# Performance work log

Hardware: AMD Instinct MI355X
Metric: run time of the kernel (lower is better)

## Reference

```python
import jax, jax.numpy as jnp
import numpy as np

N = 4096      # n_nodes
F = 512       # input_dim
R = 64        # repr_dim
H = 8         # n_heads
EPS_BIAS = 0.01
ALPHA = 0.2   # LeakyReLU negative slope
NEG_BIG = 1e16


def setup_inputs() -> dict:
    key = jax.random.key(0)
    k1, k2, k3, k4, k5 = jax.random.split(key, 5)
    node_matrix = jax.random.normal(k1, (N, F), dtype=jnp.float32)
    adjacency_matrix = (jax.random.uniform(k2, (N, N)) < 0.01).astype(jnp.float32)
    adjacency_matrix = jnp.maximum(adjacency_matrix, jnp.eye(N, dtype=jnp.float32))
    # learned parameters (xavier-ish scale)
    W = jax.random.normal(k3, (H, F, R), dtype=jnp.float32) * 0.06
    shared_attention = jax.random.normal(k4, (H, 2 * R), dtype=jnp.float32) * 0.1
    attention_biases = jax.random.normal(k5, (N, N), dtype=jnp.float32) * 0.02
    return {
        "node_matrix": node_matrix,
        "adjacency_matrix": adjacency_matrix,
        "W": W,
        "shared_attention": shared_attention,
        "attention_biases": attention_biases,
    }


def reference(node_matrix, adjacency_matrix, W, shared_attention, attention_biases):
    # hidden_repr: [H, N, R]
    hidden = jnp.einsum('nf,hfr->hnr', node_matrix, W)
    # per-head source/destination scores: [H, N]
    a_src = jnp.einsum('hnr,hr->hn', hidden, shared_attention[:, :R])
    a_dst = jnp.einsum('hnr,hr->hn', hidden, shared_attention[:, R:])
    # broadcast-sum + trainable pair bias: [H, N, N]
    pre = a_src[:, :, None] + a_dst[:, None, :] + EPS_BIAS * attention_biases[None]
    full = jnp.where(pre >= 0, pre, ALPHA * pre)  # LeakyReLU
    # adjacency masking then row softmax
    scores = full + (-NEG_BIG * (1.0 - adjacency_matrix))[None]
    att = jax.nn.softmax(scores, axis=-1)  # [H, N, N]
    # weighted aggregation: [H, N, R]
    out = jnp.einsum('hnm,hmr->hnr', att, hidden)
    # 'concat' aggregation: [N, H*R], head h occupies columns h*R:(h+1)*R
    return jnp.transpose(out, (1, 0, 2)).reshape(N, H * R)
```

## Files before the change

kernel.cpp:

```cpp
#include <hip/hip_runtime.h>
#include <hip/hip_bf16.h>

#define NN 4096
#define FF 512
#define RR 64
#define HH 8
#define HR (HH * RR)
#define CAP 128
#define ATT_STRIDE 144

typedef short bf16x8 __attribute__((ext_vector_type(8)));
typedef float f32x4 __attribute__((ext_vector_type(4)));

__device__ __forceinline__ unsigned short f2bf(float f) {
  __hip_bfloat16 h = __float2bfloat16(f);
  return *reinterpret_cast<unsigned short*>(&h);
}
__device__ __forceinline__ float bf2f(unsigned short u) {
  union { unsigned u32; float f; } cv;
  cv.u32 = ((unsigned)u) << 16;
  return cv.f;
}
__device__ __forceinline__ unsigned nib4(const float4 v) {
  unsigned m = 0;
  if (v.x != 0.f) m |= 1u;
  if (v.y != 0.f) m |= 2u;
  if (v.z != 0.f) m |= 4u;
  if (v.w != 0.f) m |= 8u;
  return m;
}

__global__ __launch_bounds__(256) void k_stream(
    const float* __restrict__ X, const float* __restrict__ W,
    const float* __restrict__ adj,
    unsigned short* __restrict__ Xb, unsigned short* __restrict__ BbT,
    int* __restrict__ colsG, int* __restrict__ cnts)
{
  __shared__ unsigned short wt[64][68];
  const int b = blockIdx.x;
  const int tid = threadIdx.x;

  if (b < 1024) {
    const int lane = tid & 63;
    const int row = b * 4 + (tid >> 6);
    const float* arow = adj + (size_t)row * NN;
    unsigned long long pm = 0;
    {
      float4 buf[8];
#pragma unroll
      for (int c = 0; c < 8; ++c)
        buf[c] = *reinterpret_cast<const float4*>(&arow[c * 256 + (lane << 2)]);
#pragma unroll
      for (int c = 0; c < 8; ++c)
        pm |= (unsigned long long)nib4(buf[c]) << (4 * c);
#pragma unroll
      for (int c = 0; c < 8; ++c)
        buf[c] = *reinterpret_cast<const float4*>(&arow[(c + 8) * 256 + (lane << 2)]);
#pragma unroll
      for (int c = 0; c < 8; ++c)
        pm |= (unsigned long long)nib4(buf[c]) << (4 * c + 32);
    }
    const int cnt = __popcll(pm);
    int pfx = cnt;
#pragma unroll
    for (int off = 1; off < 64; off <<= 1) {
      const int o = __shfl_up(pfx, off);
      if (lane >= off) pfx += o;
    }
    int pos = pfx - cnt;
    unsigned long long m = pm;
    int* cg = colsG + (size_t)row * CAP;
    while (m) {
      const int bit = (int)__builtin_ctzll(m);
      m &= m - 1;
      if (pos < CAP) cg[pos] = ((bit >> 2) << 8) + (lane << 2) + (bit & 3);
      ++pos;
    }
    const int tot = __shfl(pfx, 63);
    for (int p = tot + lane; p < CAP; p += 64) cg[p] = 0;
    if (lane == 63) cnts[row] = tot < CAP ? tot : CAP;
  } else if (b < 3072) {
    const int t = (b - 1024) * 256 + tid;
    const float4 v = reinterpret_cast<const float4*>(X)[t];
    ushort4 u;
    u.x = f2bf(v.x); u.y = f2bf(v.y); u.z = f2bf(v.z); u.w = f2bf(v.w);
    reinterpret_cast<ushort4*>(Xb)[t] = u;
  } else {
    const int b2 = b - 3072;
    const int h = b2 >> 3;
    const int f0 = (b2 & 7) << 6;
    const int fr = tid >> 2;
    const int rq = (tid & 3) << 4;
    const float* wp = W + (size_t)h * FF * RR + (size_t)(f0 + fr) * RR + rq;
#pragma unroll
    for (int v = 0; v < 4; ++v) {
      const float4 x = *reinterpret_cast<const float4*>(wp + v * 4);
      wt[rq + v * 4 + 0][fr] = f2bf(x.x);
      wt[rq + v * 4 + 1][fr] = f2bf(x.y);
      wt[rq + v * 4 + 2][fr] = f2bf(x.z);
      wt[rq + v * 4 + 3][fr] = f2bf(x.w);
    }
    __syncthreads();
    const int r = tid >> 2;
    unsigned short* op = BbT + (size_t)(h * 64 + r) * FF + f0 + ((tid & 3) << 4);
    int4 w0 = *reinterpret_cast<const int4*>(&wt[r][(tid & 3) << 4]);
    int4 w1 = *reinterpret_cast<const int4*>(&wt[r][((tid & 3) << 4) + 8]);
    *reinterpret_cast<int4*>(op) = w0;
    *reinterpret_cast<int4*>(op + 8) = w1;
  }
}

__global__ __launch_bounds__(256) void k_gemm_hidden(
    const unsigned short* __restrict__ Xb,
    const unsigned short* __restrict__ BbT,
    const float* __restrict__ sa,
    unsigned short* __restrict__ hiddenT,
    float* __restrict__ a_srcT,
    float* __restrict__ a_dstT)
{
  const int row0 = blockIdx.x * 64;
  const int h = blockIdx.y;
  const int n0 = h * 64;
  __shared__ unsigned short Als[64 * 32];
  __shared__ unsigned short Bls[64 * 32];
  __shared__ float redS[64][2];
  __shared__ float redD[64][2];
  const int tid = threadIdx.x;
  const int l = tid & 63;
  const int wid = tid >> 6;
  const int wr = wid >> 1, wc = wid & 1;

  f32x4 acc[2][2];
#pragma unroll
  for (int a = 0; a < 2; ++a)
#pragma unroll
    for (int bb = 0; bb < 2; ++bb) acc[a][bb] = (f32x4){0.f, 0.f, 0.f, 0.f};

  const int srow = tid >> 2;
  const int skel = (tid & 3) * 8;

  for (int k0 = 0; k0 < FF; k0 += 32) {
    const int4 av = *reinterpret_cast<const int4*>(
        &Xb[(size_t)(row0 + srow) * FF + k0 + skel]);
    const int4 bv = *reinterpret_cast<const int4*>(
        &BbT[(size_t)(n0 + srow) * FF + k0 + skel]);
    __syncthreads();
    *reinterpret_cast<int4*>(&Als[tid * 8]) = av;
    *reinterpret_cast<int4*>(&Bls[tid * 8]) = bv;
    __syncthreads();

    const int ka = (l >> 4) * 8;
    const bf16x8 a0 = *reinterpret_cast<const bf16x8*>(&Als[(32 * wr + 0  + (l & 15)) * 32 + ka]);
    const bf16x8 a1 = *reinterpret_cast<const bf16x8*>(&Als[(32 * wr + 16 + (l & 15)) * 32 + ka]);
    const bf16x8 b0 = *reinterpret_cast<const bf16x8*>(&Bls[(32 * wc + 0  + (l & 15)) * 32 + ka]);
    const bf16x8 b1 = *reinterpret_cast<const bf16x8*>(&Bls[(32 * wc + 16 + (l & 15)) * 32 + ka]);
    acc[0][0] = __builtin_amdgcn_mfma_f32_16x16x32_bf16(a0, b0, acc[0][0], 0, 0, 0);
    acc[0][1] = __builtin_amdgcn_mfma_f32_16x16x32_bf16(a0, b1, acc[0][1], 0, 0, 0);
    acc[1][0] = __builtin_amdgcn_mfma_f32_16x16x32_bf16(a1, b0, acc[1][0], 0, 0, 0);
    acc[1][1] = __builtin_amdgcn_mfma_f32_16x16x32_bf16(a1, b1, acc[1][1], 0, 0, 0);
  }

  const int lg = l >> 4;
  const int lc = l & 15;

#pragma unroll
  for (int mi = 0; mi < 2; ++mi)
#pragma unroll
    for (int ni = 0; ni < 2; ++ni)
#pragma unroll
      for (int j = 0; j < 4; ++j) {
        const int rowg = row0 + 32 * wr + 16 * mi + (lg << 2) + j;
        const int colg = n0 + 32 * wc + 16 * ni + lc;
        hiddenT[(size_t)rowg * HR + colg] = f2bf(acc[mi][ni][j]);
      }

  float sS[2], sD[2];
#pragma unroll
  for (int ni = 0; ni < 2; ++ni) {
    const int col = 32 * wc + 16 * ni + lc;
    sS[ni] = sa[(size_t)h * 2 * RR + col];
    sD[ni] = sa[(size_t)h * 2 * RR + RR + col];
  }
#pragma unroll
  for (int mi = 0; mi < 2; ++mi)
#pragma unroll
    for (int j = 0; j < 4; ++j) {
      float ps = acc[mi][0][j] * sS[0] + acc[mi][1][j] * sS[1];
      float pd = acc[mi][0][j] * sD[0] + acc[mi][1][j] * sD[1];
#pragma unroll
      for (int off = 8; off >= 1; off >>= 1) {
        ps += __shfl_xor(ps, off);
        pd += __shfl_xor(pd, off);
      }
      if (lc == 0) {
        const int rl = 32 * wr + 16 * mi + (lg << 2) + j;
        redS[rl][wc] = ps;
        redD[rl][wc] = pd;
      }
    }
  __syncthreads();
  if (tid < 64) {
    a_srcT[(size_t)(row0 + tid) * HH + h] = redS[tid][0] + redS[tid][1];
    a_dstT[(size_t)(row0 + tid) * HH + h] = redD[tid][0] + redD[tid][1];
  }
}

__global__ __launch_bounds__(256) void k_gat_row(
    const int* __restrict__ colsG,
    const int* __restrict__ cnts,
    const float* __restrict__ bias,
    const float* __restrict__ a_srcT,
    const float* __restrict__ a_dstT,
    const unsigned short* __restrict__ hiddenT,
    float* __restrict__ out)
{
  const int i = blockIdx.x;
  const int tid = threadIdx.x;

  __shared__ __align__(16) float att[HH][ATT_STRIDE];
  __shared__ int cols[CAP];
  __shared__ __align__(16) float accred[4][HR];

  int c = 0;
  float4 d0, d1;
  float b = 0.f;
  if (tid < CAP) {
    c = colsG[(size_t)i * CAP + tid];
  }
  const int count = cnts[i];
  if (tid < CAP) {
    b = 0.01f * bias[(size_t)i * NN + c];
    d0 = *reinterpret_cast<const float4*>(&a_dstT[(size_t)c * HH]);
    d1 = *reinterpret_cast<const float4*>(&a_dstT[(size_t)c * HH + 4]);
  }
  const float4 s0 = *reinterpret_cast<const float4*>(&a_srcT[(size_t)i * HH]);
  const float4 s1 = *reinterpret_cast<const float4*>(&a_srcT[(size_t)i * HH + 4]);

  if (tid < CAP) {
    cols[tid] = c;
    float s;
    s = s0.x + d0.x + b; att[0][tid] = (s >= 0.f) ? s : 0.2f * s;
    s = s0.y + d0.y + b; att[1][tid] = (s >= 0.f) ? s : 0.2f * s;
    s = s0.z + d0.z + b; att[2][tid] = (s >= 0.f) ? s : 0.2f * s;
    s = s0.w + d0.w + b; att[3][tid] = (s >= 0.f) ? s : 0.2f * s;
    s = s1.x + d1.x + b; att[4][tid] = (s >= 0.f) ? s : 0.2f * s;
    s = s1.y + d1.y + b; att[5][tid] = (s >= 0.f) ? s : 0.2f * s;
    s = s1.z + d1.z + b; att[6][tid] = (s >= 0.f) ? s : 0.2f * s;
    s = s1.w + d1.w + b; att[7][tid] = (s >= 0.f) ? s : 0.2f * s;
  }
  __syncthreads();

  {
    const int g = tid >> 5;
    const int l = tid & 31;
    float* arow_h = att[g];
    float m = -3.0e38f;
    for (int t = l; t < count; t += 32) m = fmaxf(m, arow_h[t]);
#pragma unroll
    for (int o = 16; o >= 1; o >>= 1) m = fmaxf(m, __shfl_xor(m, o));
    float ssum = 0.f;
    for (int t = l; t < count; t += 32) {
      const float e = expf(arow_h[t] - m);
      arow_h[t] = e;
      ssum += e;
    }
#pragma unroll
    for (int o = 16; o >= 1; o >>= 1) ssum += __shfl_xor(ssum, o);
    const float inv = 1.0f / ssum;
    for (int t = l; t < count; t += 32) arow_h[t] *= inv;
  }
  __syncthreads();

  {
    const int g2 = tid >> 6;
    const int o0 = (tid & 63) << 3;
    const float* attrow = att[o0 >> 6];
    const unsigned short* hb = hiddenT + o0;
    const int q = (count + 3) >> 2;
    const int t0 = g2 * q;
    const int t1 = min(t0 + q, count);
    float4 accA = make_float4(0.f, 0.f, 0.f, 0.f);
    float4 accB = make_float4(0.f, 0.f, 0.f, 0.f);
    for (int t = t0; t < t1; ++t) {
      const int cc = cols[t];
      const float a = attrow[t];
      const ushort4 ua = *reinterpret_cast<const ushort4*>(hb + (size_t)cc * HR);
      const ushort4 ub = *reinterpret_cast<const ushort4*>(hb + (size_t)cc * HR + 4);
      accA.x += a * bf2f(ua.x); accA.y += a * bf2f(ua.y);
      accA.z += a * bf2f(ua.z); accA.w += a * bf2f(ua.w);
      accB.x += a * bf2f(ub.x); accB.y += a * bf2f(ub.y);
      accB.z += a * bf2f(ub.z); accB.w += a * bf2f(ub.w);
    }
    *reinterpret_cast<float4*>(&accred[g2][o0]) = accA;
    *reinterpret_cast<float4*>(&accred[g2][o0 + 4]) = accB;
  }
  __syncthreads();
  {
    const int o = tid << 1;
    const float2 r = make_float2(
        accred[0][o] + accred[1][o] + accred[2][o] + accred[3][o],
        accred[0][o + 1] + accred[1][o + 1] + accred[2][o + 1] + accred[3][o + 1]);
    *reinterpret_cast<float2*>(&out[(size_t)i * HR + o]) = r;
  }
}

extern "C" void kernel_launch(void* const* d_in, const int* in_sizes, int n_in,
                              void* d_out, int out_size, void* d_ws, size_t ws_size,
                              hipStream_t stream) {
  const float* X    = (const float*)d_in[0];
  const float* adj  = (const float*)d_in[1];
  const float* W    = (const float*)d_in[2];
  const float* sa   = (const float*)d_in[3];
  const float* bias = (const float*)d_in[4];
  float* out = (float*)d_out;

  unsigned short* hiddenT = (unsigned short*)d_ws;
  unsigned short* Xb  = hiddenT + (size_t)NN * HR;
  unsigned short* BbT = Xb + (size_t)NN * FF;
  float* a_srcT = (float*)(BbT + (size_t)HR * FF);
  float* a_dstT = a_srcT + (size_t)NN * HH;
  int* cnts     = (int*)(a_dstT + (size_t)NN * HH);
  int* colsG    = cnts + NN;

  k_stream<<<dim3(3136), 256, 0, stream>>>(X, W, adj, Xb, BbT, colsG, cnts);
  k_gemm_hidden<<<dim3(NN / 64, HH), 256, 0, stream>>>(Xb, BbT, sa, hiddenT, a_srcT, a_dstT);
  k_gat_row<<<dim3(NN), 256, 0, stream>>>(colsG, cnts, bias, a_srcT, a_dstT, hiddenT, out);
}
```

Before: 47.00 us.

## Double-buffer GEMM loads, nontemporal adjacency loads, widen gather and register softmax

The hidden GEMM now double-buffers its LDS tiles and prefetches the next K-slice into registers, so the per-iteration barriers drop from two to one. Adjacency scanning uses nontemporal loads to avoid cache pollution. The aggregation splits the neighbor list 8 ways with 16 contiguous bf16 per thread, giving wider loads. The softmax keeps values in registers and uses the fast __expf. Trade-offs are more LDS (a larger accred array and doubled tiles), more registers, and a slightly less accurate exp.

```diff
diff --git a/kernel.cpp b/kernel.cpp
--- a/kernel.cpp
+++ b/kernel.cpp
@@ -7,7 +7,7 @@
 #define HH 8
 #define HR (HH * RR)
 #define CAP 128
-#define ATT_STRIDE 144
+#define ATT_STRIDE 132
 
 typedef short bf16x8 __attribute__((ext_vector_type(8)));
 typedef float f32x4 __attribute__((ext_vector_type(4)));
@@ -20,6 +20,16 @@
   union { unsigned u32; float f; } cv;
   cv.u32 = ((unsigned)u) << 16;
   return cv.f;
+}
+__device__ __forceinline__ float lo2f(int w) {
+  union { int i; float f; } c; c.i = w << 16; return c.f;
+}
+__device__ __forceinline__ float hi2f(int w) {
+  union { int i; float f; } c; c.i = w & 0xffff0000; return c.f;
+}
+__device__ __forceinline__ float4 ntload4(const float* p) {
+  const f32x4 v = __builtin_nontemporal_load(reinterpret_cast<const f32x4*>(p));
+  return make_float4(v.x, v.y, v.z, v.w);
 }
 __device__ __forceinline__ unsigned nib4(const float4 v) {
   unsigned m = 0;
@@ -49,13 +59,13 @@
       float4 buf[8];
 #pragma unroll
       for (int c = 0; c < 8; ++c)
-        buf[c] = *reinterpret_cast<const float4*>(&arow[c * 256 + (lane << 2)]);
+        buf[c] = ntload4(&arow[c * 256 + (lane << 2)]);
 #pragma unroll
       for (int c = 0; c < 8; ++c)
         pm |= (unsigned long long)nib4(buf[c]) << (4 * c);
 #pragma unroll
       for (int c = 0; c < 8; ++c)
-        buf[c] = *reinterpret_cast<const float4*>(&arow[(c + 8) * 256 + (lane << 2)]);
+        buf[c] = ntload4(&arow[(c + 8) * 256 + (lane << 2)]);
 #pragma unroll
       for (int c = 0; c < 8; ++c)
         pm |= (unsigned long long)nib4(buf[c]) << (4 * c + 32);
@@ -121,8 +131,8 @@
   const int row0 = blockIdx.x * 64;
   const int h = blockIdx.y;
   const int n0 = h * 64;
-  __shared__ unsigned short Als[64 * 32];
-  __shared__ unsigned short Bls[64 * 32];
+  __shared__ unsigned short Als[2][64 * 32];
+  __shared__ unsigned short Bls[2][64 * 32];
   __shared__ float redS[64][2];
   __shared__ float redD[64][2];
   const int tid = threadIdx.x;
@@ -138,26 +148,31 @@
 
   const int srow = tid >> 2;
   const int skel = (tid & 3) * 8;
-
+  const unsigned short* xp = &Xb[(size_t)(row0 + srow) * FF + skel];
+  const unsigned short* bp = &BbT[(size_t)(n0 + srow) * FF + skel];
+
+  int4 av = *reinterpret_cast<const int4*>(xp);
+  int4 bv = *reinterpret_cast<const int4*>(bp);
+
+  int cur = 0;
   for (int k0 = 0; k0 < FF; k0 += 32) {
-    const int4 av = *reinterpret_cast<const int4*>(
-        &Xb[(size_t)(row0 + srow) * FF + k0 + skel]);
-    const int4 bv = *reinterpret_cast<const int4*>(
-        &BbT[(size_t)(n0 + srow) * FF + k0 + skel]);
+    *reinterpret_cast<int4*>(&Als[cur][tid * 8]) = av;
+    *reinterpret_cast<int4*>(&Bls[cur][tid * 8]) = bv;
     __syncthreads();
-    *reinterpret_cast<int4*>(&Als[tid * 8]) = av;
-    *reinterpret_cast<int4*>(&Bls[tid * 8]) = bv;
-    __syncthreads();
-
+    if (k0 + 32 < FF) {
+      av = *reinterpret_cast<const int4*>(xp + k0 + 32);
+      bv = *reinterpret_cast<const int4*>(bp + k0 + 32);
+    }
     const int ka = (l >> 4) * 8;
-    const bf16x8 a0 = *reinterpret_cast<const bf16x8*>(&Als[(32 * wr + 0  + (l & 15)) * 32 + ka]);
-    const bf16x8 a1 = *reinterpret_cast<const bf16x8*>(&Als[(32 * wr + 16 + (l & 15)) * 32 + ka]);
-    const bf16x8 b0 = *reinterpret_cast<const bf16x8*>(&Bls[(32 * wc + 0  + (l & 15)) * 32 + ka]);
-    const bf16x8 b1 = *reinterpret_cast<const bf16x8*>(&Bls[(32 * wc + 16 + (l & 15)) * 32 + ka]);
+    const bf16x8 a0 = *reinterpret_cast<const bf16x8*>(&Als[cur][(32 * wr + 0  + (l & 15)) * 32 + ka]);
+    const bf16x8 a1 = *reinterpret_cast<const bf16x8*>(&Als[cur][(32 * wr + 16 + (l & 15)) * 32 + ka]);
+    const bf16x8 b0 = *reinterpret_cast<const bf16x8*>(&Bls[cur][(32 * wc + 0  + (l & 15)) * 32 + ka]);
+    const bf16x8 b1 = *reinterpret_cast<const bf16x8*>(&Bls[cur][(32 * wc + 16 + (l & 15)) * 32 + ka]);
     acc[0][0] = __builtin_amdgcn_mfma_f32_16x16x32_bf16(a0, b0, acc[0][0], 0, 0, 0);
     acc[0][1] = __builtin_amdgcn_mfma_f32_16x16x32_bf16(a0, b1, acc[0][1], 0, 0, 0);
     acc[1][0] = __builtin_amdgcn_mfma_f32_16x16x32_bf16(a1, b0, acc[1][0], 0, 0, 0);
     acc[1][1] = __builtin_amdgcn_mfma_f32_16x16x32_bf16(a1, b1, acc[1][1], 0, 0, 0);
+    cur ^= 1;
   }
 
   const int lg = l >> 4;
@@ -219,14 +234,12 @@
 
   __shared__ __align__(16) float att[HH][ATT_STRIDE];
   __shared__ int cols[CAP];
-  __shared__ __align__(16) float accred[4][HR];
+  __shared__ __align__(16) float accred[8][HR];
 
   int c = 0;
   float4 d0, d1;
   float b = 0.f;
-  if (tid < CAP) {
-    c = colsG[(size_t)i * CAP + tid];
-  }
+  if (tid < CAP) c = colsG[(size_t)i * CAP + tid];
   const int count = cnts[i];
   if (tid < CAP) {
     b = 0.01f * bias[(size_t)i * NN + c];
@@ -253,54 +266,72 @@
   {
     const int g = tid >> 5;
     const int l = tid & 31;
-    float* arow_h = att[g];
-    float m = -3.0e38f;
-    for (int t = l; t < count; t += 32) m = fmaxf(m, arow_h[t]);
+    float v[4];
+#pragma unroll
+    for (int j = 0; j < 4; ++j) {
+      const int t = l + j * 32;
+      v[j] = (t < count) ? att[g][t] : -3.0e38f;
+    }
+    float m = fmaxf(fmaxf(v[0], v[1]), fmaxf(v[2], v[3]));
 #pragma unroll
     for (int o = 16; o >= 1; o >>= 1) m = fmaxf(m, __shfl_xor(m, o));
+    float e[4];
     float ssum = 0.f;
-    for (int t = l; t < count; t += 32) {
-      const float e = expf(arow_h[t] - m);
-      arow_h[t] = e;
-      ssum += e;
+#pragma unroll
+    for (int j = 0; j < 4; ++j) {
+      e[j] = __expf(v[j] - m);
+      ssum += e[j];
     }
 #pragma unroll
     for (int o = 16; o >= 1; o >>= 1) ssum += __shfl_xor(ssum, o);
     const float inv = 1.0f / ssum;
-    for (int t = l; t < count; t += 32) arow_h[t] *= inv;
+#pragma unroll
+    for (int j = 0; j < 4; ++j) att[g][l + j * 32] = e[j] * inv;
   }
   __syncthreads();
 
   {
-    const int g2 = tid >> 6;
-    const int o0 = (tid & 63) << 3;
+    const int g2 = tid >> 5;
+    const int o0 = (tid & 31) << 4;
     const float* attrow = att[o0 >> 6];
     const unsigned short* hb = hiddenT + o0;
-    const int q = (count + 3) >> 2;
+    const int q = (count + 7) >> 3;
     const int t0 = g2 * q;
     const int t1 = min(t0 + q, count);
-    float4 accA = make_float4(0.f, 0.f, 0.f, 0.f);
-    float4 accB = make_float4(0.f, 0.f, 0.f, 0.f);
+    float acc[16];
+#pragma unroll
+    for (int j = 0; j < 16; ++j) acc[j] = 0.f;
     for (int t = t0; t < t1; ++t) {
       const int cc = cols[t];
       const float a = attrow[t];
-      const ushort4 ua = *reinterpret_cast<const ushort4*>(hb + (size_t)cc * HR);
-      const ushort4 ub = *reinterpret_cast<const ushort4*>(hb + (size_t)cc * HR + 4);
-      accA.x += a * bf2f(ua.x); accA.y += a * bf2f(ua.y);
-      accA.z += a * bf2f(ua.z); accA.w += a * bf2f(ua.w);
-      accB.x += a * bf2f(ub.x); accB.y += a * bf2f(ub.y);
-      accB.z += a * bf2f(ub.z); accB.w += a * bf2f(ub.w);
-    }
-    *reinterpret_cast<float4*>(&accred[g2][o0]) = accA;
-    *reinterpret_cast<float4*>(&accred[g2][o0 + 4]) = accB;
+      const unsigned short* hp = hb + (size_t)cc * HR;
+      const int4 u0 = *reinterpret_cast<const int4*>(hp);
+      const int4 u1 = *reinterpret_cast<const int4*>(hp + 8);
+      acc[0]  += a * lo2f(u0.x); acc[1]  += a * hi2f(u0.x);
+      acc[2]  += a * lo2f(u0.y); acc[3]  += a * hi2f(u0.y);
+      acc[4]  += a * lo2f(u0.z); acc[5]  += a * hi2f(u0.z);
+      acc[6]  += a * lo2f(u0.w); acc[7]  += a * hi2f(u0.w);
+      acc[8]  += a * lo2f(u1.x); acc[9]  += a * hi2f(u1.x);
+      acc[10] += a * lo2f(u1.y); acc[11] += a * hi2f(u1.y);
+      acc[12] += a * lo2f(u1.z); acc[13] += a * hi2f(u1.z);
+      acc[14] += a * lo2f(u1.w); acc[15] += a * hi2f(u1.w);
+    }
+#pragma unroll
+    for (int j = 0; j < 4; ++j) {
+      float4 v = make_float4(acc[j * 4], acc[j * 4 + 1], acc[j * 4 + 2], acc[j * 4 + 3]);
+      *reinterpret_cast<float4*>(&accred[g2][o0 + j * 4]) = v;
+    }
   }
   __syncthreads();
   {
     const int o = tid << 1;
-    const float2 r = make_float2(
-        accred[0][o] + accred[1][o] + accred[2][o] + accred[3][o],
-        accred[0][o + 1] + accred[1][o + 1] + accred[2][o + 1] + accred[3][o + 1]);
-    *reinterpret_cast<float2*>(&out[(size_t)i * HR + o]) = r;
+    float r0 = 0.f, r1 = 0.f;
+#pragma unroll
+    for (int g = 0; g < 8; ++g) {
+      const float2 v = *reinterpret_cast<const float2*>(&accred[g][o]);
+      r0 += v.x; r1 += v.y;
+    }
+    *reinterpret_cast<float2*>(&out[(size_t)i * HR + o]) = make_float2(r0, r1);
   }
 }
 
```

Result: slower. 49.99 us (+6.4%).
